# Performance work log

Hardware: AMD Instinct MI355X
Metric: run time of the kernel (lower is better)

Reference implementation:

```python
import jax, jax.numpy as jnp
import numpy as np

IGNORE_INDEX = -100


def setup_inputs() -> dict:
    key = jax.random.key(0)
    k1, k2, k3 = jax.random.split(key, 3)
    B, S, D, V = 4, 2048, 2048, 32000
    hidden_states = jax.random.normal(k1, (B, S, D), dtype=jnp.float32)
    lm_head_weight = jax.random.normal(k2, (V, D), dtype=jnp.float32) * (D ** -0.5)
    labels = jax.random.randint(k3, (B, S), 0, V, dtype=jnp.int64)
    return {"hidden_states": hidden_states, "lm_head_weight": lm_head_weight, "labels": labels}


def reference(hidden_states, lm_head_weight, labels):
    D = hidden_states.shape[-1]
    # causal LM shift: predict token t+1 from hidden state t
    h = hidden_states[..., :-1, :].astype(jnp.float32).reshape(-1, D)   # [N, D]
    t = labels[..., 1:].reshape(-1)                                     # [N]
    w = lm_head_weight.astype(jnp.float32)                              # [V, D]

    logits = jnp.einsum("nd,vd->nv", h, w)                              # [N, V]
    lse = jax.nn.logsumexp(logits, axis=-1)                             # [N]

    valid = t != IGNORE_INDEX
    safe_t = jnp.where(valid, t, 0)
    gold = jnp.take_along_axis(logits, safe_t[:, None], axis=-1)[:, 0]  # [N]

    nll = jnp.where(valid, lse - gold, 0.0)
    n_valid = jnp.maximum(jnp.sum(valid.astype(jnp.float32)), 1.0)
    return jnp.sum(nll) / n_valid
```

## Files before the change

### kernel.cpp

```cpp
#include <hip/hip_runtime.h>
#include <stdint.h>

#define IGNORE_INDEX (-100)

typedef __attribute__((ext_vector_type(8))) short bf16x8;
typedef __attribute__((ext_vector_type(4))) float f32x4;

static constexpr int Bv = 4, Sv = 2048, Dv = 2048, Vv = 32000;
static constexpr int Nv = Bv * (Sv - 1);
static constexpr int NP = 8192;
static constexpr int BM = 256;
static constexpr int BK = 64;
static constexpr int NT = Dv / BK;

typedef const __attribute__((address_space(1))) unsigned int* gptr_t;
typedef __attribute__((address_space(3))) unsigned int* lptr_t;

__device__ __forceinline__ unsigned short f2bf(float f) {
    unsigned int u = __float_as_uint(f);
    u += 0x7fffu + ((u >> 16) & 1u);
    return (unsigned short)(u >> 16);
}

__global__ void convert_w_kernel(const float* __restrict__ w,
                                 unsigned short* __restrict__ wbf) {
    int i = blockIdx.x * blockDim.x + threadIdx.x;
    const float4 v = ((const float4*)w)[i];
    ushort4 o;
    o.x = f2bf(v.x); o.y = f2bf(v.y); o.z = f2bf(v.z); o.w = f2bf(v.w);
    ((ushort4*)wbf)[i] = o;
}

__global__ void convert_h_kernel(const float* __restrict__ h,
                                 unsigned short* __restrict__ hbf) {
    int i = blockIdx.x * blockDim.x + threadIdx.x;
    int e0 = i * 4;
    int n = e0 >> 11;
    int d = e0 & 2047;
    ushort4 o;
    if (n < Nv) {
        int b = n / 2047;
        int s = n - b * 2047;
        const float4 v = *(const float4*)(h + ((size_t)b * Sv + s) * Dv + d);
        o.x = f2bf(v.x); o.y = f2bf(v.y); o.z = f2bf(v.z); o.w = f2bf(v.w);
    } else {
        o.x = 0; o.y = 0; o.z = 0; o.w = 0;
    }
    ((ushort4*)hbf)[i] = o;
}

__global__ void prep_meta_kernel(const int* __restrict__ labels,
                                 int* __restrict__ t,
                                 float* __restrict__ sumexp,
                                 float* __restrict__ gold) {
    int n = blockIdx.x * blockDim.x + threadIdx.x;
    if (n >= NP) return;
    sumexp[n] = 0.0f;
    gold[n] = 0.0f;
    int tv = IGNORE_INDEX;
    if (n < Nv) {
        int b = n / 2047;
        int s = n - b * 2047;
        tv = labels[b * Sv + s + 1];
    }
    t[n] = tv;
}

__global__ __launch_bounds__(512, 2)
void ce_gemm(const unsigned short* __restrict__ hbf,
             const unsigned short* __restrict__ wbf,
             const int* __restrict__ t,
             float* __restrict__ sumexp,
             float* __restrict__ gold) {
    __shared__ unsigned short lds_a[2][BM * BK];
    __shared__ unsigned short lds_b[2][BM * BK];
    __shared__ float lds_rowsum[BM];
    __shared__ int lds_t[BM];

    const int tid  = threadIdx.x;
    const int lane = tid & 63;
    const int wave = tid >> 6;
    const int wr   = wave >> 2;
    const int wc   = wave & 3;
    const int quad = lane >> 4;
    const int l15  = lane & 15;
    const int R0   = blockIdx.x * BM;
    const int C0   = blockIdx.y * BM;

    f32x4 acc[8][4];
    const f32x4 z = {0.f, 0.f, 0.f, 0.f};
#pragma unroll
    for (int mi = 0; mi < 8; ++mi)
#pragma unroll
        for (int ni = 0; ni < 4; ++ni)
            acc[mi][ni] = z;

    const int ld_r = tid >> 3;
    const int jg   = (tid & 7) ^ (ld_r & 7);
    const unsigned short* ga = hbf + (size_t)(R0 + ld_r) * Dv + jg * 8;
    const unsigned short* gb = wbf + (size_t)(C0 + ld_r) * Dv + jg * 8;

#define STAGE(kt, buf)                                                         \
    do {                                                                       \
        const int _k0 = (kt) * BK;                                             \
        unsigned short* _la = &lds_a[(buf)][tid * 8];                          \
        unsigned short* _lb = &lds_b[(buf)][tid * 8];                          \
        _Pragma("unroll")                                                      \
        for (int _i = 0; _i < 4; ++_i) {                                       \
            __builtin_amdgcn_global_load_lds(                                  \
                (gptr_t)(ga + (size_t)_i * 64 * Dv + _k0),                     \
                (lptr_t)(_la + _i * 4096), 16, 0, 0);                          \
            __builtin_amdgcn_global_load_lds(                                  \
                (gptr_t)(gb + (size_t)_i * 64 * Dv + _k0),                     \
                (lptr_t)(_lb + _i * 4096), 16, 0, 0);                          \
        }                                                                      \
    } while (0)

    STAGE(0, 0);
    STAGE(1, 1);
    asm volatile("s_waitcnt vmcnt(8)" ::: "memory");
    __builtin_amdgcn_s_barrier();

    int cur = 0;
    for (int kt = 0; kt < NT; ++kt) {
        const unsigned short* ba = &lds_a[cur][0];
        const unsigned short* bb = &lds_b[cur][0];

        bf16x8 bfr[4][2];
#pragma unroll
        for (int ni = 0; ni < 4; ++ni) {
            const int brow = wc * 64 + ni * 16 + l15;
            const int sw = brow & 7;
            bfr[ni][0] = *(const bf16x8*)(bb + brow * BK + ((quad ^ sw) * 8));
            bfr[ni][1] = *(const bf16x8*)(bb + brow * BK + (((quad + 4) ^ sw) * 8));
        }

        __builtin_amdgcn_s_setprio(1);
#pragma unroll
        for (int mi = 0; mi < 8; ++mi) {
            const int arow = wr * 128 + mi * 16 + l15;
            const int sw = arow & 7;
            bf16x8 a0 = *(const bf16x8*)(ba + arow * BK + ((quad ^ sw) * 8));
            bf16x8 a1 = *(const bf16x8*)(ba + arow * BK + (((quad + 4) ^ sw) * 8));
#pragma unroll
            for (int ni = 0; ni < 4; ++ni)
                acc[mi][ni] = __builtin_amdgcn_mfma_f32_16x16x32_bf16(
                    a0, bfr[ni][0], acc[mi][ni], 0, 0, 0);
#pragma unroll
            for (int ni = 0; ni < 4; ++ni)
                acc[mi][ni] = __builtin_amdgcn_mfma_f32_16x16x32_bf16(
                    a1, bfr[ni][1], acc[mi][ni], 0, 0, 0);
        }
        __builtin_amdgcn_s_setprio(0);

        asm volatile("s_waitcnt lgkmcnt(0)" ::: "memory");
        __builtin_amdgcn_s_barrier();

        if (kt + 2 < NT) {
            STAGE(kt + 2, cur);
            asm volatile("s_waitcnt vmcnt(8)" ::: "memory");
        } else if (kt + 1 < NT) {
            asm volatile("s_waitcnt vmcnt(0)" ::: "memory");
        }
        __builtin_amdgcn_s_barrier();
        cur ^= 1;
    }
#undef STAGE

    __syncthreads();
    if (tid < BM) {
        lds_rowsum[tid] = 0.0f;
        lds_t[tid] = t[R0 + tid];
    }
    __syncthreads();

#pragma unroll
    for (int mi = 0; mi < 8; ++mi) {
#pragma unroll
        for (int reg = 0; reg < 4; ++reg) {
            const int lrow = wr * 128 + mi * 16 + quad * 4 + reg;
            const int grow = R0 + lrow;
            const int lbl  = lds_t[lrow];
            float s = 0.0f;
#pragma unroll
            for (int ni = 0; ni < 4; ++ni) {
                const float v = acc[mi][ni][reg];
                s += __expf(v);
                const int gcol = C0 + wc * 64 + ni * 16 + l15;
                if (lbl == gcol) gold[grow] = v;
            }
#pragma unroll
            for (int off = 1; off < 16; off <<= 1)
                s += __shfl_xor(s, off, 64);
            if (l15 == 0) atomicAdd(&lds_rowsum[lrow], s);
        }
    }
    __syncthreads();
    if (tid < BM) {
        const int grow = R0 + tid;
        if (grow < Nv) atomicAdd(&sumexp[grow], lds_rowsum[tid]);
    }
}

__global__ void ce_finalize(const float* __restrict__ sumexp,
                            const float* __restrict__ gold,
                            const int* __restrict__ t,
                            float* __restrict__ out) {
    __shared__ float ssum[4];
    __shared__ float scnt[4];
    float s = 0.0f, cnt = 0.0f;
    for (int n = threadIdx.x; n < Nv; n += 256) {
        if (t[n] != IGNORE_INDEX) {
            s += logf(sumexp[n]) - gold[n];
            cnt += 1.0f;
        }
    }
#pragma unroll
    for (int off = 32; off > 0; off >>= 1) {
        s += __shfl_down(s, off, 64);
        cnt += __shfl_down(cnt, off, 64);
    }
    const int wid = threadIdx.x >> 6;
    if ((threadIdx.x & 63) == 0) { ssum[wid] = s; scnt[wid] = cnt; }
    __syncthreads();
    if (threadIdx.x == 0) {
        float S = 0.0f, C = 0.0f;
        for (int i = 0; i < 4; ++i) { S += ssum[i]; C += scnt[i]; }
        out[0] = S / fmaxf(C, 1.0f);
    }
}

extern "C" void kernel_launch(void* const* d_in, const int* in_sizes, int n_in,
                              void* d_out, int out_size, void* d_ws, size_t ws_size,
                              hipStream_t stream) {
    const float* h      = (const float*)d_in[0];
    const float* w      = (const float*)d_in[1];
    const int*   labels = (const int*)d_in[2];
    float* out = (float*)d_out;

    char* ws = (char*)d_ws;
    unsigned short* hbf = (unsigned short*)ws;
    unsigned short* wbf = (unsigned short*)(ws + (size_t)NP * Dv * 2);
    char* tail = ws + (size_t)NP * Dv * 2 + (size_t)Vv * Dv * 2;
    float* sumexp = (float*)tail;
    float* gold   = (float*)(tail + (size_t)NP * 4);
    int*   t      = (int*)(tail + (size_t)NP * 8);

    hipLaunchKernelGGL(convert_w_kernel, dim3((Vv * Dv / 4) / 256), dim3(256), 0, stream, w, wbf);
    hipLaunchKernelGGL(convert_h_kernel, dim3((NP * Dv / 4) / 256), dim3(256), 0, stream, h, hbf);
    hipLaunchKernelGGL(prep_meta_kernel, dim3(NP / 256), dim3(256), 0, stream, labels, t, sumexp, gold);
    hipLaunchKernelGGL(ce_gemm, dim3(NP / BM, Vv / BM), dim3(512), 0, stream,
                       hbf, wbf, t, sumexp, gold);
    hipLaunchKernelGGL(ce_finalize, dim3(1), dim3(256), 0, stream, sumexp, gold, t, out);
}
```

Baseline: 1.597 ms.

## Split K-loop into eight interleaved phases with fine-grained half-tile global-to-LDS prefetch

Measured after the change: 1.392 ms. 1.15x faster.

```diff
diff --git a/kernel.cpp b/kernel.cpp
--- a/kernel.cpp
+++ b/kernel.cpp
@@ -100,74 +100,107 @@
     const unsigned short* ga = hbf + (size_t)(R0 + ld_r) * Dv + jg * 8;
     const unsigned short* gb = wbf + (size_t)(C0 + ld_r) * Dv + jg * 8;
 
-#define STAGE(kt, buf)                                                         \
-    do {                                                                       \
-        const int _k0 = (kt) * BK;                                             \
-        unsigned short* _la = &lds_a[(buf)][tid * 8];                          \
-        unsigned short* _lb = &lds_b[(buf)][tid * 8];                          \
-        _Pragma("unroll")                                                      \
-        for (int _i = 0; _i < 4; ++_i) {                                       \
-            __builtin_amdgcn_global_load_lds(                                  \
-                (gptr_t)(ga + (size_t)_i * 64 * Dv + _k0),                     \
-                (lptr_t)(_la + _i * 4096), 16, 0, 0);                          \
-            __builtin_amdgcn_global_load_lds(                                  \
-                (gptr_t)(gb + (size_t)_i * 64 * Dv + _k0),                     \
-                (lptr_t)(_lb + _i * 4096), 16, 0, 0);                          \
-        }                                                                      \
+#define STAGE_HALF(DSTARR, GBASE, KT, H)                                    \
+    do {                                                                    \
+        _Pragma("unroll")                                                   \
+        for (int _i = 2 * (H); _i < 2 * (H) + 2; ++_i) {                    \
+            __builtin_amdgcn_global_load_lds(                               \
+                (gptr_t)((GBASE) + (size_t)_i * 64 * Dv + (KT) * BK),       \
+                (lptr_t)(&DSTARR[tid * 8 + _i * 4096]), 16, 0, 0);          \
+        }                                                                   \
     } while (0)
 
-    STAGE(0, 0);
-    STAGE(1, 1);
-    asm volatile("s_waitcnt vmcnt(8)" ::: "memory");
+#define LDSF(BASE, R, C) \
+    (*(const bf16x8*)((BASE) + (R) * BK + (((C) ^ ((R) & 7)) * 8)))
+
+#define VM6 asm volatile("s_waitcnt vmcnt(6)" ::: "memory")
+#define VM0 asm volatile("s_waitcnt vmcnt(0)" ::: "memory")
+#define NOVM ((void)0)
+
+#define PHASE(ABUF, Q, LOADB, BBUF, VMW, ...)                               \
+    do {                                                                    \
+        bf16x8 a0_, a1_, a2_, a3_;                                          \
+        {                                                                   \
+            const int r0_ = (2 * (Q)) * 32 + wr * 16 + l15;                 \
+            const int r1_ = (2 * (Q) + 1) * 32 + wr * 16 + l15;             \
+            const unsigned short* ab_ = &lds_a[ABUF][0];                    \
+            a0_ = LDSF(ab_, r0_, quad);                                     \
+            a1_ = LDSF(ab_, r0_, quad + 4);                                 \
+            a2_ = LDSF(ab_, r1_, quad);                                     \
+            a3_ = LDSF(ab_, r1_, quad + 4);                                 \
+        }                                                                   \
+        if (LOADB) {                                                        \
+            const unsigned short* bb_ = &lds_b[BBUF][0];                    \
+            _Pragma("unroll")                                               \
+            for (int ni_ = 0; ni_ < 4; ++ni_) {                             \
+                const int br_ = wc * 64 + ni_ * 16 + l15;                   \
+                bfr[ni_][0] = LDSF(bb_, br_, quad);                         \
+                bfr[ni_][1] = LDSF(bb_, br_, quad + 4);                     \
+            }                                                               \
+        }                                                                   \
+        __VA_ARGS__;                                                        \
+        __builtin_amdgcn_s_barrier();                                       \
+        asm volatile("s_waitcnt lgkmcnt(0)" ::: "memory");                  \
+        __builtin_amdgcn_sched_barrier(0);                                  \
+        __builtin_amdgcn_s_setprio(1);                                      \
+        {                                                                   \
+            const int miA_ = 2 * (Q), miB_ = 2 * (Q) + 1;                   \
+            _Pragma("unroll")                                               \
+            for (int ni_ = 0; ni_ < 4; ++ni_) {                             \
+                acc[miA_][ni_] = __builtin_amdgcn_mfma_f32_16x16x32_bf16(   \
+                    a0_, bfr[ni_][0], acc[miA_][ni_], 0, 0, 0);             \
+                acc[miA_][ni_] = __builtin_amdgcn_mfma_f32_16x16x32_bf16(   \
+                    a1_, bfr[ni_][1], acc[miA_][ni_], 0, 0, 0);             \
+            }                                                               \
+            _Pragma("unroll")                                               \
+            for (int ni_ = 0; ni_ < 4; ++ni_) {                             \
+                acc[miB_][ni_] = __builtin_amdgcn_mfma_f32_16x16x32_bf16(   \
+                    a2_, bfr[ni_][0], acc[miB_][ni_], 0, 0, 0);             \
+                acc[miB_][ni_] = __builtin_amdgcn_mfma_f32_16x16x32_bf16(   \
+                    a3_, bfr[ni_][1], acc[miB_][ni_], 0, 0, 0);             \
+            }                                                               \
+        }                                                                   \
+        __builtin_amdgcn_s_setprio(0);                                      \
+        VMW;                                                                \
+        __builtin_amdgcn_s_barrier();                                       \
+    } while (0)
+
+    bf16x8 bfr[4][2];
+
+    STAGE_HALF(lds_a[0], ga, 0, 0);
+    STAGE_HALF(lds_a[0], ga, 0, 1);
+    STAGE_HALF(lds_b[0], gb, 0, 0);
+    STAGE_HALF(lds_b[0], gb, 0, 1);
+    STAGE_HALF(lds_b[1], gb, 1, 0);
+    STAGE_HALF(lds_b[1], gb, 1, 1);
+    STAGE_HALF(lds_a[1], ga, 1, 0);
+    VM6;
     __builtin_amdgcn_s_barrier();
 
-    int cur = 0;
-    for (int kt = 0; kt < NT; ++kt) {
-        const unsigned short* ba = &lds_a[cur][0];
-        const unsigned short* bb = &lds_b[cur][0];
-
-        bf16x8 bfr[4][2];
-#pragma unroll
-        for (int ni = 0; ni < 4; ++ni) {
-            const int brow = wc * 64 + ni * 16 + l15;
-            const int sw = brow & 7;
-            bfr[ni][0] = *(const bf16x8*)(bb + brow * BK + ((quad ^ sw) * 8));
-            bfr[ni][1] = *(const bf16x8*)(bb + brow * BK + (((quad + 4) ^ sw) * 8));
-        }
-
-        __builtin_amdgcn_s_setprio(1);
-#pragma unroll
-        for (int mi = 0; mi < 8; ++mi) {
-            const int arow = wr * 128 + mi * 16 + l15;
-            const int sw = arow & 7;
-            bf16x8 a0 = *(const bf16x8*)(ba + arow * BK + ((quad ^ sw) * 8));
-            bf16x8 a1 = *(const bf16x8*)(ba + arow * BK + (((quad + 4) ^ sw) * 8));
-#pragma unroll
-            for (int ni = 0; ni < 4; ++ni)
-                acc[mi][ni] = __builtin_amdgcn_mfma_f32_16x16x32_bf16(
-                    a0, bfr[ni][0], acc[mi][ni], 0, 0, 0);
-#pragma unroll
-            for (int ni = 0; ni < 4; ++ni)
-                acc[mi][ni] = __builtin_amdgcn_mfma_f32_16x16x32_bf16(
-                    a1, bfr[ni][1], acc[mi][ni], 0, 0, 0);
-        }
-        __builtin_amdgcn_s_setprio(0);
-
-        asm volatile("s_waitcnt lgkmcnt(0)" ::: "memory");
-        __builtin_amdgcn_s_barrier();
-
-        if (kt + 2 < NT) {
-            STAGE(kt + 2, cur);
-            asm volatile("s_waitcnt vmcnt(8)" ::: "memory");
-        } else if (kt + 1 < NT) {
-            asm volatile("s_waitcnt vmcnt(0)" ::: "memory");
-        }
-        __builtin_amdgcn_s_barrier();
-        cur ^= 1;
-    }
-#undef STAGE
-
-    __syncthreads();
+#pragma unroll 1
+    for (int j = 0; j < 15; ++j) {
+        const int t1 = 2 * j + 1, t2 = 2 * j + 2, t3 = 2 * j + 3;
+        PHASE(0, 0, 1, 0, NOVM, STAGE_HALF(lds_a[1], ga, t1, 1));
+        PHASE(0, 1, 0, 0, NOVM, STAGE_HALF(lds_b[0], gb, t2, 0));
+        PHASE(0, 2, 0, 0, NOVM, STAGE_HALF(lds_b[0], gb, t2, 1));
+        PHASE(0, 3, 0, 0, VM6,  STAGE_HALF(lds_a[0], ga, t2, 0));
+        PHASE(1, 0, 1, 1, NOVM, STAGE_HALF(lds_a[0], ga, t2, 1));
+        PHASE(1, 1, 0, 1, NOVM, STAGE_HALF(lds_b[1], gb, t3, 0));
+        PHASE(1, 2, 0, 1, NOVM, STAGE_HALF(lds_b[1], gb, t3, 1));
+        PHASE(1, 3, 0, 1, VM6,  STAGE_HALF(lds_a[1], ga, t3, 0));
+    }
+    PHASE(0, 0, 1, 0, NOVM, STAGE_HALF(lds_a[1], ga, 31, 1));
+    PHASE(0, 1, 0, 0, NOVM, NOVM);
+    PHASE(0, 2, 0, 0, NOVM, NOVM);
+    PHASE(0, 3, 0, 0, VM0,  NOVM);
+    PHASE(1, 0, 1, 1, NOVM, NOVM);
+    PHASE(1, 1, 0, 1, NOVM, NOVM);
+    PHASE(1, 2, 0, 1, NOVM, NOVM);
+    PHASE(1, 3, 0, 1, NOVM, NOVM);
+
+#undef PHASE
+#undef STAGE_HALF
+
     if (tid < BM) {
         lds_rowsum[tid] = 0.0f;
         lds_t[tid] = t[R0 + tid];
@@ -178,7 +211,7 @@
     for (int mi = 0; mi < 8; ++mi) {
 #pragma unroll
         for (int reg = 0; reg < 4; ++reg) {
-            const int lrow = wr * 128 + mi * 16 + quad * 4 + reg;
+            const int lrow = mi * 32 + wr * 16 + quad * 4 + reg;
             const int grow = R0 + lrow;
             const int lbl  = lds_t[lrow];
             float s = 0.0f;
```
